# Performance work log

Measured on AMD Instinct MI355X. Metric: run time of the kernel, lower is better.

## Reference

```python
import jax, jax.numpy as jnp
import numpy as np

N_NODES = 100000
N_EDGES = 1600000
F_IN = 128
HIDDEN = 64
N_CLASSES = 32


def setup_inputs() -> dict:
    key = jax.random.key(0)
    k1, k2, k3, k4 = jax.random.split(key, 4)
    x = jax.random.normal(k1, (N_NODES, F_IN), dtype=jnp.float32)
    edge_index = jax.random.randint(k2, (2, N_EDGES), 0, N_NODES, dtype=jnp.int32)
    # Glorot-style init for the two GCNConv weight matrices
    W1 = jax.random.normal(k3, (F_IN, HIDDEN), dtype=jnp.float32) * (1.0 / np.sqrt(F_IN))
    W2 = jax.random.normal(k4, (HIDDEN, N_CLASSES), dtype=jnp.float32) * (1.0 / np.sqrt(HIDDEN))
    b1 = jnp.zeros((HIDDEN,), dtype=jnp.float32)
    b2 = jnp.zeros((N_CLASSES,), dtype=jnp.float32)
    return {"x": x, "edge_index": edge_index, "W1": W1, "b1": b1, "W2": W2, "b2": b2}


def gcn_conv(x, W, b, src, dst, num_nodes):
    # PyG GCNConv: linear transform first, then normalized neighbor aggregation.
    h = x @ W  # [N, out]
    ones = jnp.ones(src.shape, dtype=h.dtype)
    deg = jax.ops.segment_sum(ones, dst, num_segments=num_nodes)  # in-degree incl. self-loops
    d_inv_sqrt = jnp.where(deg > 0, jax.lax.rsqrt(deg), 0.0)
    norm = d_inv_sqrt[src] * d_inv_sqrt[dst]  # [E]
    msg = h[src] * norm[:, None]              # gather + scale, [E, out]
    out = jax.ops.segment_sum(msg, dst, num_segments=num_nodes)  # scatter-add
    return out + b


def reference(x, edge_index, W1, b1, W2, b2):
    n = x.shape[0]
    # add_self_loops=True (GCNConv default)
    loop = jnp.arange(n, dtype=edge_index.dtype)
    src = jnp.concatenate([edge_index[0], loop])
    dst = jnp.concatenate([edge_index[1], loop])
    h = jax.nn.relu(gcn_conv(x, W1, b1, src, dst, n))
    # F.dropout(training=self.training) is identity in eval mode
    logits = gcn_conv(h, W2, b2, src, dst, n)
    return jax.nn.log_softmax(logits, axis=1)
```

## Files before the change

### kernel.cpp

```cpp
#include <hip/hip_runtime.h>

#define F_IN 128
#define HID 64
#define CLS 32
#define BCAP 8192

typedef short v8s __attribute__((ext_vector_type(8)));
typedef float f4 __attribute__((ext_vector_type(4)));
typedef float f2 __attribute__((ext_vector_type(2)));

__device__ __forceinline__ float bflo(unsigned int w) { return __uint_as_float(w << 16); }
__device__ __forceinline__ float bfhi(unsigned int w) { return __uint_as_float(w & 0xFFFF0000u); }
__device__ __forceinline__ unsigned short f2bf(float f) {
    unsigned int u = __float_as_uint(f);
    u += 0x7FFFu + ((u >> 16) & 1u);
    return (unsigned short)(u >> 16);
}
__device__ __forceinline__ unsigned int pack2(float lo, float hi) {
    unsigned int r;
    asm("v_cvt_pk_bf16_f32 %0, %1, %2" : "=v"(r) : "v"(lo), "v"(hi));
    return r;
}
__device__ __forceinline__ unsigned char f2fp8(float v) {
    return (unsigned char)(__builtin_amdgcn_cvt_pk_fp8_f32(v, v, 0, false) & 0xFF);
}

__global__ __launch_bounds__(256) void k_front(const int* __restrict__ src,
                                               const int* __restrict__ dst,
                                               int* __restrict__ bC,
                                               int* __restrict__ bucketed,
                                               const float* __restrict__ x,
                                               const float* __restrict__ W1,
                                               unsigned char* __restrict__ y,
                                               int E, int nb, int n, int sB) {
    __shared__ union {
        struct { int h[512]; int chunk[512]; } sc;
        unsigned short w1[HID * 136];
    } S;
    int tid = threadIdx.x;
    int bid = blockIdx.x;

    if (bid < sB) {
        for (int i = tid; i < nb; i += 256) S.sc.h[i] = 0;
        __syncthreads();
        int e0 = bid << 11;
        int myRec[8], myB[8], myRank[8];
#pragma unroll
        for (int k = 0; k < 8; ++k) {
            int e = e0 + k * 256 + tid;
            if (e < E) {
                int d = dst[e];
                myB[k] = d >> 8;
                myRec[k] = src[e] | ((d & 255) << 17);
                myRank[k] = atomicAdd(&S.sc.h[myB[k]], 1);
            } else {
                myB[k] = -1;
            }
        }
        __syncthreads();
        for (int i = tid; i < nb; i += 256)
            S.sc.chunk[i] = S.sc.h[i] ? (i * BCAP + atomicAdd(&bC[i], S.sc.h[i])) : 0;
        __syncthreads();
#pragma unroll
        for (int k = 0; k < 8; ++k)
            if (myB[k] >= 0) bucketed[S.sc.chunk[myB[k]] + myRank[k]] = myRec[k];
    } else {
        for (int i = tid; i < F_IN * HID; i += 256) {
            int k = i >> 6, nn = i & 63;
            S.w1[nn * 136 + k] = f2bf(W1[i]);
        }
        __syncthreads();
        int lane = tid & 63;
        int quad = lane >> 4, c = lane & 15;
        int nstripes = (n + 15) >> 4;
        int stripe = (bid - sB) * 4 + (tid >> 6);
        if (stripe >= nstripes) return;
        int row0 = stripe << 4;

        f4 acc[4] = {};
        union { unsigned int u[4]; v8s v; } au;
#pragma unroll
        for (int ks = 0; ks < 4; ++ks) {
            int k0 = ks * 32 + quad * 8;
            int row = row0 + c;
            if (row >= n) row = n - 1;
            const float* xp = x + (size_t)row * F_IN + k0;
            float4 lo = *(const float4*)xp;
            float4 hi = *(const float4*)(xp + 4);
            au.u[0] = pack2(lo.x, lo.y);
            au.u[1] = pack2(lo.z, lo.w);
            au.u[2] = pack2(hi.x, hi.y);
            au.u[3] = pack2(hi.z, hi.w);
            v8s a = au.v;
#pragma unroll
            for (int nt = 0; nt < 4; ++nt) {
                v8s bb = *(const v8s*)&S.w1[(nt * 16 + c) * 136 + k0];
                acc[nt] = __builtin_amdgcn_mfma_f32_16x16x32_bf16(a, bb, acc[nt], 0, 0, 0);
            }
        }
#pragma unroll
        for (int reg = 0; reg < 4; ++reg) {
            int row = row0 + quad * 4 + reg;
            if (row < n) {
#pragma unroll
                for (int nt = 0; nt < 4; ++nt)
                    y[(size_t)row * HID + nt * 16 + c] = f2fp8(acc[nt][reg]);
            }
        }
    }
}

__global__ __launch_bounds__(512) void k_csr(const int* __restrict__ bC,
                                             const int* __restrict__ bucketed,
                                             int* __restrict__ pk,
                                             float* __restrict__ dinv, int* __restrict__ csr,
                                             int n) {
    __shared__ int cnt[256];
    __shared__ int s[256];
    __shared__ int baseS[256];
    int b = blockIdx.x;
    int node0 = b << 8;
    int tid = threadIdx.x;
    if (tid < 256) cnt[tid] = 0;
    __syncthreads();
    int p0 = b * BCAP, p1 = p0 + bC[b];

    int rec[16], rnk[16];
#pragma unroll
    for (int k = 0; k < 16; ++k) {
        int p = p0 + tid + (k << 9);
        if (p < p1) {
            int r = bucketed[p];
            rec[k] = r;
            rnk[k] = atomicAdd(&cnt[r >> 17], 1);
        } else {
            rec[k] = -1;
        }
    }
    __syncthreads();
    int v = 0;
    if (tid < 256) { v = cnt[tid]; s[tid] = v; }
    __syncthreads();
    for (int off = 1; off < 256; off <<= 1) {
        int t = (tid >= off && tid < 256) ? s[tid - off] : 0;
        __syncthreads();
        if (tid < 256) s[tid] += t;
        __syncthreads();
    }
    if (tid < 256) {
        int myoff = p0 + s[tid] - v;
        baseS[tid] = myoff;
        int node = node0 + tid;
        if (node < n) {
            pk[node] = myoff | (v << 22);
            dinv[node] = rsqrtf((float)(v + 1));
        }
    }
    __syncthreads();
#pragma unroll
    for (int k = 0; k < 16; ++k) {
        if (rec[k] >= 0) csr[baseS[rec[k] >> 17] + rnk[k]] = rec[k] & 0x1FFFF;
    }
}

__global__ __launch_bounds__(256) void k_gather64_w2(const int* __restrict__ pk,
                                                     const int* __restrict__ csr,
                                                     const unsigned char* __restrict__ xw8,
                                                     const float* __restrict__ b1,
                                                     const float* __restrict__ W2,
                                                     const float* __restrict__ dinv,
                                                     unsigned short* __restrict__ y2, int n) {
    __shared__ unsigned short Wt[CLS * 72];
    __shared__ unsigned short Hl[32 * 72];
    int tid = threadIdx.x;
    for (int i = tid; i < HID * CLS; i += 256) {
        int k = i >> 5, nn = i & 31;
        Wt[nn * 72 + k] = f2bf(W2[i]);
    }

    int g = tid >> 3;
    int l = tid & 7;
    int node = blockIdx.x * 32 + g;

    if (node < n) {
        unsigned int pv = (unsigned int)pk[node];
        int p0 = pv & 0x3FFFFF;
        int cntv = (int)(pv >> 22);
        int p1 = p0 + cntv;
        float dd = rsqrtf((float)(cntv + 1));
        uint2 sw = *(const uint2*)(xw8 + (size_t)node * HID + l * 8);

        f2 a0 = {0.f, 0.f}, a1 = a0, a2 = a0, a3 = a0;
        f2 c0 = a0, c1 = a0, c2 = a0, c3 = a0;
        int q = p0;
        for (; q + 3 < p1; q += 4) {
            int s0 = csr[q], s1 = csr[q + 1], s2 = csr[q + 2], s3 = csr[q + 3];
            float d0 = dinv[s0], d1 = dinv[s1], d2 = dinv[s2], d3 = dinv[s3];
            uint2 w0 = *(const uint2*)(xw8 + (size_t)s0 * HID + l * 8);
            uint2 w1 = *(const uint2*)(xw8 + (size_t)s1 * HID + l * 8);
            uint2 w2 = *(const uint2*)(xw8 + (size_t)s2 * HID + l * 8);
            uint2 w3 = *(const uint2*)(xw8 + (size_t)s3 * HID + l * 8);
            f2 D0 = {d0, d0}, D1 = {d1, d1}, D2 = {d2, d2}, D3 = {d3, d3};
            a0 += __builtin_amdgcn_cvt_pk_f32_fp8(w0.x, false) * D0;
            a1 += __builtin_amdgcn_cvt_pk_f32_fp8(w0.x, true) * D0;
            a2 += __builtin_amdgcn_cvt_pk_f32_fp8(w0.y, false) * D0;
            a3 += __builtin_amdgcn_cvt_pk_f32_fp8(w0.y, true) * D0;
            c0 += __builtin_amdgcn_cvt_pk_f32_fp8(w1.x, false) * D1;
            c1 += __builtin_amdgcn_cvt_pk_f32_fp8(w1.x, true) * D1;
            c2 += __builtin_amdgcn_cvt_pk_f32_fp8(w1.y, false) * D1;
            c3 += __builtin_amdgcn_cvt_pk_f32_fp8(w1.y, true) * D1;
            a0 += __builtin_amdgcn_cvt_pk_f32_fp8(w2.x, false) * D2;
            a1 += __builtin_amdgcn_cvt_pk_f32_fp8(w2.x, true) * D2;
            a2 += __builtin_amdgcn_cvt_pk_f32_fp8(w2.y, false) * D2;
            a3 += __builtin_amdgcn_cvt_pk_f32_fp8(w2.y, true) * D2;
            c0 += __builtin_amdgcn_cvt_pk_f32_fp8(w3.x, false) * D3;
            c1 += __builtin_amdgcn_cvt_pk_f32_fp8(w3.x, true) * D3;
            c2 += __builtin_amdgcn_cvt_pk_f32_fp8(w3.y, false) * D3;
            c3 += __builtin_amdgcn_cvt_pk_f32_fp8(w3.y, true) * D3;
        }
        for (; q < p1; ++q) {
            int s0 = csr[q];
            float d0 = dinv[s0];
            uint2 w0 = *(const uint2*)(xw8 + (size_t)s0 * HID + l * 8);
            f2 D0 = {d0, d0};
            a0 += __builtin_amdgcn_cvt_pk_f32_fp8(w0.x, false) * D0;
            a1 += __builtin_amdgcn_cvt_pk_f32_fp8(w0.x, true) * D0;
            a2 += __builtin_amdgcn_cvt_pk_f32_fp8(w0.y, false) * D0;
            a3 += __builtin_amdgcn_cvt_pk_f32_fp8(w0.y, true) * D0;
        }
        a0 += c0; a1 += c1; a2 += c2; a3 += c3;
        f2 DS = {dd, dd};
        a0 += __builtin_amdgcn_cvt_pk_f32_fp8(sw.x, false) * DS;
        a1 += __builtin_amdgcn_cvt_pk_f32_fp8(sw.x, true) * DS;
        a2 += __builtin_amdgcn_cvt_pk_f32_fp8(sw.y, false) * DS;
        a3 += __builtin_amdgcn_cvt_pk_f32_fp8(sw.y, true) * DS;

        float4 bb0 = *(const float4*)(b1 + l * 8);
        float4 bb1 = *(const float4*)(b1 + l * 8 + 4);
        float h0 = fmaxf(a0.x * dd + bb0.x, 0.f);
        float h1 = fmaxf(a0.y * dd + bb0.y, 0.f);
        float h2 = fmaxf(a1.x * dd + bb0.z, 0.f);
        float h3 = fmaxf(a1.y * dd + bb0.w, 0.f);
        float h4 = fmaxf(a2.x * dd + bb1.x, 0.f);
        float h5 = fmaxf(a2.y * dd + bb1.y, 0.f);
        float h6 = fmaxf(a3.x * dd + bb1.z, 0.f);
        float h7 = fmaxf(a3.y * dd + bb1.w, 0.f);
        uint4 hp;
        hp.x = pack2(h0, h1);
        hp.y = pack2(h2, h3);
        hp.z = pack2(h4, h5);
        hp.w = pack2(h6, h7);
        *(uint4*)&Hl[g * 72 + l * 8] = hp;
    }
    __syncthreads();

    int wv = tid >> 6;
    int t = wv & 1, nt = wv >> 1;
    int lane = tid & 63, quad = lane >> 4, c = lane & 15;
    f4 acc = {};
#pragma unroll
    for (int ks = 0; ks < 2; ++ks) {
        int k0 = ks * 32 + quad * 8;
        v8s aF = *(const v8s*)&Hl[(t * 16 + c) * 72 + k0];
        v8s bF = *(const v8s*)&Wt[(nt * 16 + c) * 72 + k0];
        acc = __builtin_amdgcn_mfma_f32_16x16x32_bf16(aF, bF, acc, 0, 0, 0);
    }
    int row0 = blockIdx.x * 32 + t * 16;
#pragma unroll
    for (int reg = 0; reg < 4; ++reg) {
        int row = row0 + quad * 4 + reg;
        if (row < n) {
            float dd2 = dinv[row];
            y2[(size_t)row * CLS + nt * 16 + c] = f2bf(acc[reg] * dd2);
        }
    }
}

__global__ __launch_bounds__(256) void k_gather32_lsm(const int* __restrict__ pk,
                                                      const int* __restrict__ csr,
                                                      const unsigned short* __restrict__ hwb,
                                                      const float* __restrict__ b,
                                                      float* __restrict__ out, int n) {
    int tid = threadIdx.x;
    int node = blockIdx.x * 64 + (tid >> 2);
    if (node >= n) return;
    int l = tid & 3;
    unsigned int pv = (unsigned int)pk[node];
    int p0 = pv & 0x3FFFFF;
    int cntv = (int)(pv >> 22);
    int p1 = p0 + cntv;
    float dd = rsqrtf((float)(cntv + 1));
    uint4 sw = *(const uint4*)(hwb + (size_t)node * CLS + l * 8);

    float A0 = 0.f, A1 = 0.f, A2 = 0.f, A3 = 0.f, A4 = 0.f, A5 = 0.f, A6 = 0.f, A7 = 0.f;
    float B0 = 0.f, B1 = 0.f, B2 = 0.f, B3 = 0.f, B4 = 0.f, B5 = 0.f, B6 = 0.f, B7 = 0.f;
    int p = p0;
    for (; p + 3 < p1; p += 4) {
        int s0 = csr[p], s1 = csr[p + 1], s2 = csr[p + 2], s3 = csr[p + 3];
        uint4 w0 = *(const uint4*)(hwb + (size_t)s0 * CLS + l * 8);
        uint4 w1 = *(const uint4*)(hwb + (size_t)s1 * CLS + l * 8);
        uint4 w2 = *(const uint4*)(hwb + (size_t)s2 * CLS + l * 8);
        uint4 w3 = *(const uint4*)(hwb + (size_t)s3 * CLS + l * 8);
        A0 += bflo(w0.x); A1 += bfhi(w0.x); A2 += bflo(w0.y); A3 += bfhi(w0.y);
        A4 += bflo(w0.z); A5 += bfhi(w0.z); A6 += bflo(w0.w); A7 += bfhi(w0.w);
        B0 += bflo(w1.x); B1 += bfhi(w1.x); B2 += bflo(w1.y); B3 += bfhi(w1.y);
        B4 += bflo(w1.z); B5 += bfhi(w1.z); B6 += bflo(w1.w); B7 += bfhi(w1.w);
        A0 += bflo(w2.x); A1 += bfhi(w2.x); A2 += bflo(w2.y); A3 += bfhi(w2.y);
        A4 += bflo(w2.z); A5 += bfhi(w2.z); A6 += bflo(w2.w); A7 += bfhi(w2.w);
        B0 += bflo(w3.x); B1 += bfhi(w3.x); B2 += bflo(w3.y); B3 += bfhi(w3.y);
        B4 += bflo(w3.z); B5 += bfhi(w3.z); B6 += bflo(w3.w); B7 += bfhi(w3.w);
    }
    for (; p < p1; ++p) {
        int s0 = csr[p];
        uint4 w0 = *(const uint4*)(hwb + (size_t)s0 * CLS + l * 8);
        A0 += bflo(w0.x); A1 += bfhi(w0.x); A2 += bflo(w0.y); A3 += bfhi(w0.y);
        A4 += bflo(w0.z); A5 += bfhi(w0.z); A6 += bflo(w0.w); A7 += bfhi(w0.w);
    }
    A0 += B0; A1 += B1; A2 += B2; A3 += B3;
    A4 += B4; A5 += B5; A6 += B6; A7 += B7;

    float4 bb0 = *(const float4*)(b + l * 8);
    float4 bb1 = *(const float4*)(b + l * 8 + 4);
    float v0 = (A0 + bflo(sw.x)) * dd + bb0.x;
    float v1 = (A1 + bfhi(sw.x)) * dd + bb0.y;
    float v2 = (A2 + bflo(sw.y)) * dd + bb0.z;
    float v3 = (A3 + bfhi(sw.y)) * dd + bb0.w;
    float v4 = (A4 + bflo(sw.z)) * dd + bb1.x;
    float v5 = (A5 + bfhi(sw.z)) * dd + bb1.y;
    float v6 = (A6 + bflo(sw.w)) * dd + bb1.z;
    float v7 = (A7 + bfhi(sw.w)) * dd + bb1.w;

    float m = fmaxf(fmaxf(fmaxf(v0, v1), fmaxf(v2, v3)), fmaxf(fmaxf(v4, v5), fmaxf(v6, v7)));
    m = fmaxf(m, __shfl_xor(m, 1));
    m = fmaxf(m, __shfl_xor(m, 2));
    float s = __expf(v0 - m) + __expf(v1 - m) + __expf(v2 - m) + __expf(v3 - m) +
              __expf(v4 - m) + __expf(v5 - m) + __expf(v6 - m) + __expf(v7 - m);
    s += __shfl_xor(s, 1);
    s += __shfl_xor(s, 2);
    float ls = m + __logf(s);
    float4 o0, o1;
    o0.x = v0 - ls; o0.y = v1 - ls; o0.z = v2 - ls; o0.w = v3 - ls;
    o1.x = v4 - ls; o1.y = v5 - ls; o1.z = v6 - ls; o1.w = v7 - ls;
    float* op = out + (size_t)node * CLS + l * 8;
    *(float4*)op = o0;
    *(float4*)(op + 4) = o1;
}

extern "C" void kernel_launch(void* const* d_in, const int* in_sizes, int n_in,
                              void* d_out, int out_size, void* d_ws, size_t ws_size,
                              hipStream_t stream) {
    const float* x  = (const float*)d_in[0];
    const int* edge = (const int*)d_in[1];
    const float* W1 = (const float*)d_in[2];
    const float* b1 = (const float*)d_in[3];
    const float* W2 = (const float*)d_in[4];
    const float* b2 = (const float*)d_in[5];
    float* out = (float*)d_out;

    int N = in_sizes[0] / F_IN;
    int E = in_sizes[1] / 2;
    const int* src = edge;
    const int* dst = edge + E;
    int NB = (N + 255) >> 8;

    float* dinv    = (float*)d_ws;
    int* pk        = (int*)(dinv + N);
    int* bC        = pk + N;
    int* csr       = bC + 512;
    int* bucketed  = csr + (size_t)NB * BCAP;
    unsigned char* bufA = (unsigned char*)(bucketed + (size_t)NB * BCAP);
    unsigned short* y2  = (unsigned short*)(bufA + (size_t)N * HID);

    hipMemsetAsync(bC, 0, (size_t)NB * sizeof(int), stream);

    int sB = (E + 2047) / 2048;
    int nstripes16 = (N + 15) >> 4;
    int gB = (nstripes16 + 3) / 4;

    k_front<<<sB + gB, 256, 0, stream>>>(src, dst, bC, bucketed, x, W1, bufA, E, NB, N, sB);

    k_csr<<<NB, 512, 0, stream>>>(bC, bucketed, pk, dinv, csr, N);

    k_gather64_w2<<<(N + 31) / 32, 256, 0, stream>>>(pk, csr, bufA, b1, W2, dinv, y2, N);

    k_gather32_lsm<<<(N + 63) / 64, 256, 0, stream>>>(pk, csr, y2, b2, out, N);
}
```

Baseline: 203.3 us.

## Pad CSR rows to 4-aligned offsets, halve bucket size, vectorize index loads

```diff
diff --git a/kernel.cpp b/kernel.cpp
--- a/kernel.cpp
+++ b/kernel.cpp
@@ -3,7 +3,7 @@
 #define F_IN 128
 #define HID 64
 #define CLS 32
-#define BCAP 8192
+#define BCAP 4096
 
 typedef short v8s __attribute__((ext_vector_type(8)));
 typedef float f4 __attribute__((ext_vector_type(4)));
@@ -34,7 +34,7 @@
                                                unsigned char* __restrict__ y,
                                                int E, int nb, int n, int sB) {
     __shared__ union {
-        struct { int h[512]; int chunk[512]; } sc;
+        struct { int h[1024]; int chunk[1024]; } sc;
         unsigned short w1[HID * 136];
     } S;
     int tid = threadIdx.x;
@@ -43,15 +43,15 @@
     if (bid < sB) {
         for (int i = tid; i < nb; i += 256) S.sc.h[i] = 0;
         __syncthreads();
-        int e0 = bid << 11;
-        int myRec[8], myB[8], myRank[8];
-#pragma unroll
-        for (int k = 0; k < 8; ++k) {
+        int e0 = bid << 12;
+        int myRec[16], myB[16], myRank[16];
+#pragma unroll
+        for (int k = 0; k < 16; ++k) {
             int e = e0 + k * 256 + tid;
             if (e < E) {
                 int d = dst[e];
-                myB[k] = d >> 8;
-                myRec[k] = src[e] | ((d & 255) << 17);
+                myB[k] = d >> 7;
+                myRec[k] = src[e] | ((d & 127) << 17);
                 myRank[k] = atomicAdd(&S.sc.h[myB[k]], 1);
             } else {
                 myB[k] = -1;
@@ -62,7 +62,7 @@
             S.sc.chunk[i] = S.sc.h[i] ? (i * BCAP + atomicAdd(&bC[i], S.sc.h[i])) : 0;
         __syncthreads();
 #pragma unroll
-        for (int k = 0; k < 8; ++k)
+        for (int k = 0; k < 16; ++k)
             if (myB[k] >= 0) bucketed[S.sc.chunk[myB[k]] + myRank[k]] = myRec[k];
     } else {
         for (int i = tid; i < F_IN * HID; i += 256) {
@@ -115,19 +115,21 @@
                                              int* __restrict__ pk,
                                              float* __restrict__ dinv, int* __restrict__ csr,
                                              int n) {
-    __shared__ int cnt[256];
-    __shared__ int s[256];
-    __shared__ int baseS[256];
+    __shared__ int cnt[128];
+    __shared__ int s[128];
+    __shared__ int baseS[128];
     int b = blockIdx.x;
-    int node0 = b << 8;
+    int node0 = b << 7;
     int tid = threadIdx.x;
-    if (tid < 256) cnt[tid] = 0;
-    __syncthreads();
-    int p0 = b * BCAP, p1 = p0 + bC[b];
-
-    int rec[16], rnk[16];
-#pragma unroll
-    for (int k = 0; k < 16; ++k) {
+    if (tid < 128) cnt[tid] = 0;
+    __syncthreads();
+    int nrec = bC[b];
+    if (nrec > BCAP) nrec = BCAP;
+    int p0 = b * BCAP, p1 = p0 + nrec;
+
+    int rec[8], rnk[8];
+#pragma unroll
+    for (int k = 0; k < 8; ++k) {
         int p = p0 + tid + (k << 9);
         if (p < p1) {
             int r = bucketed[p];
@@ -138,17 +140,17 @@
         }
     }
     __syncthreads();
-    int v = 0;
-    if (tid < 256) { v = cnt[tid]; s[tid] = v; }
-    __syncthreads();
-    for (int off = 1; off < 256; off <<= 1) {
-        int t = (tid >= off && tid < 256) ? s[tid - off] : 0;
-        __syncthreads();
-        if (tid < 256) s[tid] += t;
-        __syncthreads();
-    }
-    if (tid < 256) {
-        int myoff = p0 + s[tid] - v;
+    int v = 0, pv = 0;
+    if (tid < 128) { v = cnt[tid]; pv = (v + 3) & ~3; s[tid] = pv; }
+    __syncthreads();
+    for (int off = 1; off < 128; off <<= 1) {
+        int t = (tid >= off && tid < 128) ? s[tid - off] : 0;
+        __syncthreads();
+        if (tid < 128) s[tid] += t;
+        __syncthreads();
+    }
+    if (tid < 128) {
+        int myoff = p0 + s[tid] - pv;
         baseS[tid] = myoff;
         int node = node0 + tid;
         if (node < n) {
@@ -158,7 +160,7 @@
     }
     __syncthreads();
 #pragma unroll
-    for (int k = 0; k < 16; ++k) {
+    for (int k = 0; k < 8; ++k) {
         if (rec[k] >= 0) csr[baseS[rec[k] >> 17] + rnk[k]] = rec[k] & 0x1FFFF;
     }
 }
@@ -187,19 +189,19 @@
         int p0 = pv & 0x3FFFFF;
         int cntv = (int)(pv >> 22);
         int p1 = p0 + cntv;
-        float dd = rsqrtf((float)(cntv + 1));
+        float dd = dinv[node];
         uint2 sw = *(const uint2*)(xw8 + (size_t)node * HID + l * 8);
 
         f2 a0 = {0.f, 0.f}, a1 = a0, a2 = a0, a3 = a0;
         f2 c0 = a0, c1 = a0, c2 = a0, c3 = a0;
         int q = p0;
         for (; q + 3 < p1; q += 4) {
-            int s0 = csr[q], s1 = csr[q + 1], s2 = csr[q + 2], s3 = csr[q + 3];
-            float d0 = dinv[s0], d1 = dinv[s1], d2 = dinv[s2], d3 = dinv[s3];
-            uint2 w0 = *(const uint2*)(xw8 + (size_t)s0 * HID + l * 8);
-            uint2 w1 = *(const uint2*)(xw8 + (size_t)s1 * HID + l * 8);
-            uint2 w2 = *(const uint2*)(xw8 + (size_t)s2 * HID + l * 8);
-            uint2 w3 = *(const uint2*)(xw8 + (size_t)s3 * HID + l * 8);
+            int4 ss = *(const int4*)(csr + q);
+            float d0 = dinv[ss.x], d1 = dinv[ss.y], d2 = dinv[ss.z], d3 = dinv[ss.w];
+            uint2 w0 = *(const uint2*)(xw8 + (size_t)ss.x * HID + l * 8);
+            uint2 w1 = *(const uint2*)(xw8 + (size_t)ss.y * HID + l * 8);
+            uint2 w2 = *(const uint2*)(xw8 + (size_t)ss.z * HID + l * 8);
+            uint2 w3 = *(const uint2*)(xw8 + (size_t)ss.w * HID + l * 8);
             f2 D0 = {d0, d0}, D1 = {d1, d1}, D2 = {d2, d2}, D3 = {d3, d3};
             a0 += __builtin_amdgcn_cvt_pk_f32_fp8(w0.x, false) * D0;
             a1 += __builtin_amdgcn_cvt_pk_f32_fp8(w0.x, true) * D0;
@@ -280,6 +282,7 @@
                                                       const int* __restrict__ csr,
                                                       const unsigned short* __restrict__ hwb,
                                                       const float* __restrict__ b,
+                                                      const float* __restrict__ dinv,
                                                       float* __restrict__ out, int n) {
     int tid = threadIdx.x;
     int node = blockIdx.x * 64 + (tid >> 2);
@@ -289,18 +292,18 @@
     int p0 = pv & 0x3FFFFF;
     int cntv = (int)(pv >> 22);
     int p1 = p0 + cntv;
-    float dd = rsqrtf((float)(cntv + 1));
+    float dd = dinv[node];
     uint4 sw = *(const uint4*)(hwb + (size_t)node * CLS + l * 8);
 
     float A0 = 0.f, A1 = 0.f, A2 = 0.f, A3 = 0.f, A4 = 0.f, A5 = 0.f, A6 = 0.f, A7 = 0.f;
     float B0 = 0.f, B1 = 0.f, B2 = 0.f, B3 = 0.f, B4 = 0.f, B5 = 0.f, B6 = 0.f, B7 = 0.f;
     int p = p0;
     for (; p + 3 < p1; p += 4) {
-        int s0 = csr[p], s1 = csr[p + 1], s2 = csr[p + 2], s3 = csr[p + 3];
-        uint4 w0 = *(const uint4*)(hwb + (size_t)s0 * CLS + l * 8);
-        uint4 w1 = *(const uint4*)(hwb + (size_t)s1 * CLS + l * 8);
-        uint4 w2 = *(const uint4*)(hwb + (size_t)s2 * CLS + l * 8);
-        uint4 w3 = *(const uint4*)(hwb + (size_t)s3 * CLS + l * 8);
+        int4 ss = *(const int4*)(csr + p);
+        uint4 w0 = *(const uint4*)(hwb + (size_t)ss.x * CLS + l * 8);
+        uint4 w1 = *(const uint4*)(hwb + (size_t)ss.y * CLS + l * 8);
+        uint4 w2 = *(const uint4*)(hwb + (size_t)ss.z * CLS + l * 8);
+        uint4 w3 = *(const uint4*)(hwb + (size_t)ss.w * CLS + l * 8);
         A0 += bflo(w0.x); A1 += bfhi(w0.x); A2 += bflo(w0.y); A3 += bfhi(w0.y);
         A4 += bflo(w0.z); A5 += bfhi(w0.z); A6 += bflo(w0.w); A7 += bfhi(w0.w);
         B0 += bflo(w1.x); B1 += bfhi(w1.x); B2 += bflo(w1.y); B3 += bfhi(w1.y);
@@ -361,19 +364,19 @@
     int E = in_sizes[1] / 2;
     const int* src = edge;
     const int* dst = edge + E;
-    int NB = (N + 255) >> 8;
+    int NB = (N + 127) >> 7;
 
     float* dinv    = (float*)d_ws;
     int* pk        = (int*)(dinv + N);
     int* bC        = pk + N;
-    int* csr       = bC + 512;
+    int* csr       = bC + 1024;
     int* bucketed  = csr + (size_t)NB * BCAP;
     unsigned char* bufA = (unsigned char*)(bucketed + (size_t)NB * BCAP);
     unsigned short* y2  = (unsigned short*)(bufA + (size_t)N * HID);
 
     hipMemsetAsync(bC, 0, (size_t)NB * sizeof(int), stream);
 
-    int sB = (E + 2047) / 2048;
+    int sB = (E + 4095) / 4096;
     int nstripes16 = (N + 15) >> 4;
     int gB = (nstripes16 + 3) / 4;
 
@@ -383,5 +386,5 @@
 
     k_gather64_w2<<<(N + 31) / 32, 256, 0, stream>>>(pk, csr, bufA, b1, W2, dinv, y2, N);
 
-    k_gather32_lsm<<<(N + 63) / 64, 256, 0, stream>>>(pk, csr, y2, b2, out, N);
-}
+    k_gather32_lsm<<<(N + 63) / 64, 256, 0, stream>>>(pk, csr, y2, b2, dinv, out, N);
+}
```

After: 193.0 us. 1.05x faster.
